# Optimization experiments

Hardware: AMD Instinct MI355X
Metric: run time of the kernel (lower is better)

The kernel has to match this reference:

```python
import jax, jax.numpy as jnp
import numpy as np

B, T, C = 2, 2048, 2048
H, KVH, HD = 16, 4, 128  # heads, kv heads, head_dim
G = H // KVH             # GQA group size
THETA = 10000.0


def _rope_cos_sin(t, hd, dtype):
    inv_freq = 1.0 / (THETA ** (jnp.arange(0, hd, 2, dtype=jnp.float32) / hd))
    pos = jnp.arange(t, dtype=jnp.float32)
    freqs = pos[:, None] * inv_freq[None, :]          # [T, hd/2]
    emb = jnp.concatenate([freqs, freqs], axis=-1)    # [T, hd]
    return jnp.cos(emb).astype(dtype), jnp.sin(emb).astype(dtype)


def _rotate_half(x):
    x1, x2 = jnp.split(x, 2, axis=-1)
    return jnp.concatenate([-x2, x1], axis=-1)


def setup_inputs() -> dict:
    key = jax.random.key(0)
    ks = jax.random.split(key, 5)
    s_in = 1.0 / np.sqrt(C)
    return {
        "x": jax.random.normal(ks[0], (B, T, C), jnp.float32),
        "wq": jax.random.normal(ks[1], (C, H * HD), jnp.float32) * s_in,
        "bq": jnp.zeros((H * HD,), jnp.float32),
        "wk": jax.random.normal(ks[2], (C, KVH * HD), jnp.float32) * s_in,
        "bk": jnp.zeros((KVH * HD,), jnp.float32),
        "wv": jax.random.normal(ks[3], (C, KVH * HD), jnp.float32) * s_in,
        "bv": jnp.zeros((KVH * HD,), jnp.float32),
        "wo": jax.random.normal(ks[4], (H * HD, C), jnp.float32) * (1.0 / np.sqrt(H * HD)),
    }


def reference(x, wq, bq, wk, bk, wv, bv, wo):
    b, t, c = x.shape
    q = (x @ wq + bq).reshape(b, t, H, HD).transpose(0, 2, 1, 3)    # [B,H,T,hd]
    k = (x @ wk + bk).reshape(b, t, KVH, HD).transpose(0, 2, 1, 3)  # [B,KVH,T,hd]
    v = (x @ wv + bv).reshape(b, t, KVH, HD).transpose(0, 2, 1, 3)

    cos, sin = _rope_cos_sin(t, HD, x.dtype)  # [T,hd]
    q = q * cos + _rotate_half(q) * sin
    k = k * cos + _rotate_half(k) * sin

    # GQA: group query heads over kv heads
    qg = q.reshape(b, KVH, G, t, HD)
    scale = 1.0 / np.sqrt(HD)
    scores = jnp.einsum('bkgtd,bksd->bkgts', qg, k) * scale  # [B,KVH,G,T,T]
    causal = jnp.tril(jnp.ones((t, t), bool))
    scores = jnp.where(causal, scores, jnp.finfo(scores.dtype).min)
    attn = jax.nn.softmax(scores, axis=-1)
    out = jnp.einsum('bkgts,bksd->bkgtd', attn, v)            # [B,KVH,G,T,hd]
    out = out.reshape(b, H, t, HD).transpose(0, 2, 1, 3).reshape(b, t, H * HD)
    return out @ wo
```

## Files before the change

### kernel.cpp

```cpp
#include <hip/hip_runtime.h>
#include <hip/hip_bf16.h>
#include <math.h>

#define B_ 2
#define T_ 2048
#define C_ 2048
#define H_ 16
#define KVH_ 4
#define HD_ 128
#define G_ (H_ / KVH_)
#define MROWS (B_ * T_)
#define NQKV (H_ * HD_ + 2 * KVH_ * HD_)
#define KOFF (H_ * HD_)
#define VOFF (H_ * HD_ + KVH_ * HD_)

typedef __hip_bfloat16 bf16;
typedef short bf16x8 __attribute__((ext_vector_type(8)));
typedef short bf16x4 __attribute__((ext_vector_type(4)));
typedef float f32x4 __attribute__((ext_vector_type(4)));

__device__ __forceinline__ void gload_lds16(const void* g, void* l) {
  __builtin_amdgcn_global_load_lds(
      (const __attribute__((address_space(1))) unsigned int*)g,
      (__attribute__((address_space(3))) unsigned int*)l, 16, 0, 0);
}

static __device__ __forceinline__ f32x4 mfma32k(bf16x8 a, bf16x8 b, f32x4 c) {
  return __builtin_amdgcn_mfma_f32_16x16x32_bf16(a, b, c, 0, 0, 0);
}

static __device__ __forceinline__ f32x4 mfma16(bf16x4 a, bf16x4 b, f32x4 c) {
#if __has_builtin(__builtin_amdgcn_mfma_f32_16x16x16_bf16)
  return __builtin_amdgcn_mfma_f32_16x16x16_bf16(a, b, c, 0, 0, 0);
#else
  return __builtin_amdgcn_mfma_f32_16x16x16bf16_1k(a, b, c, 0, 0, 0);
#endif
}

static __device__ __forceinline__ short f2bf(float x) {
  unsigned u = __builtin_bit_cast(unsigned, x);
  u += 0x7FFFu + ((u >> 16) & 1u);
  return (short)(u >> 16);
}

static __device__ __forceinline__ float fexp2(float x) {
#if __has_builtin(__builtin_amdgcn_exp2f)
  return __builtin_amdgcn_exp2f(x);
#else
  return exp2f(x);
#endif
}

__global__ void cast_bf16_kernel(const float* __restrict__ in, bf16* __restrict__ out, int n) {
  int i = (blockIdx.x * 256 + threadIdx.x) * 4;
  if (i >= n) return;
  float4 v = *(const float4*)(in + i);
  out[i + 0] = __float2bfloat16(v.x);
  out[i + 1] = __float2bfloat16(v.y);
  out[i + 2] = __float2bfloat16(v.z);
  out[i + 3] = __float2bfloat16(v.w);
}

__global__ __launch_bounds__(256) void transpose_cast(const float* __restrict__ in,
                                                      bf16* __restrict__ out,
                                                      int R, int Ccols) {
  __shared__ float t[32][33];
  const int tx = threadIdx.x & 31, ty = threadIdx.x >> 5;
  const int r0 = blockIdx.y * 32, c0 = blockIdx.x * 32;
#pragma unroll
  for (int it = 0; it < 4; ++it)
    t[ty + 8 * it][tx] = in[(size_t)(r0 + ty + 8 * it) * Ccols + c0 + tx];
  __syncthreads();
#pragma unroll
  for (int it = 0; it < 4; ++it)
    out[(size_t)(c0 + ty + 8 * it) * R + r0 + tx] = __float2bfloat16(t[tx][ty + 8 * it]);
}

__global__ __launch_bounds__(256) void transpose_cast_qkvw(
    const float* __restrict__ wq, const float* __restrict__ wk,
    const float* __restrict__ wv, bf16* __restrict__ outT) {
  __shared__ float t[32][33];
  const int tx = threadIdx.x & 31, ty = threadIdx.x >> 5;
  const int r0 = blockIdx.y * 32;
  const int c0 = blockIdx.x * 32;
  const float* src;
  int nn, ld;
  if (c0 < KOFF)      { src = wq; nn = c0;        ld = 2048; }
  else if (c0 < VOFF) { src = wk; nn = c0 - KOFF; ld = 512; }
  else                { src = wv; nn = c0 - VOFF; ld = 512; }
#pragma unroll
  for (int it = 0; it < 4; ++it)
    t[ty + 8 * it][tx] = src[(size_t)(r0 + ty + 8 * it) * ld + nn + tx];
  __syncthreads();
#pragma unroll
  for (int it = 0; it < 4; ++it)
    outT[(size_t)(c0 + ty + 8 * it) * 2048 + r0 + tx] = __float2bfloat16(t[tx][ty + 8 * it]);
}

__global__ void rope_bf16(bf16* __restrict__ buf) {
  const int row = blockIdx.x / 20;
  const int hh = blockIdx.x % 20;
  const int t = row % T_;
  const int d = threadIdx.x;
  bf16* rp = buf + (size_t)row * NQKV + hh * HD_;
  float vd = __bfloat162float(rp[d]);
  float vp = __bfloat162float(rp[d ^ 64]);
  __syncthreads();
  const int i = d & 63;
  float invf = fexp2(-(float)i * (13.287712379549449f / 64.0f));
  float ang = (float)t * invf;
  float s, c;
  __sincosf(ang, &s, &c);
  rp[d] = __float2bfloat16((d < 64) ? (vd * c - vp * s) : (vd * c + vp * s));
}

__global__ __launch_bounds__(256) void pack_k(const bf16* __restrict__ qkv,
                                              bf16* __restrict__ kp) {
  const int tile = blockIdx.x & 63;
  const int bk = blockIdx.x >> 6;
  const int b = bk >> 2, kvh = bk & 3;
#pragma unroll
  for (int u = 0; u < 2; ++u) {
    const int t = threadIdx.x + u * 256;
    const int kc = t >> 6, L = t & 63;
    const bf16* src = qkv +
        (size_t)(b * T_ + tile * 32 + 16 * (kc >> 2) + (L & 15)) * NQKV +
        KOFF + kvh * HD_ + (kc & 3) * 32 + (L >> 4) * 8;
    bf16x8 v = *(const bf16x8*)src;
    *(bf16x8*)(kp + ((size_t)(bk * 64 + tile) * 8 + kc) * 512 + L * 8) = v;
  }
}

__global__ __launch_bounds__(256) void pack_v(const bf16* __restrict__ qkv,
                                              bf16* __restrict__ vp) {
  const int tile = blockIdx.x & 63;
  const int bk = blockIdx.x >> 6;
  const int b = bk >> 2, kvh = bk & 3;
#pragma unroll
  for (int u = 0; u < 2; ++u) {
    const int t = threadIdx.x + u * 256;
    const int ht = t >> 6, L = t & 63;
    const int colL = L & 15, quad = L >> 4;
    const bf16* base = qkv + (size_t)(b * T_ + tile * 32 + quad * 4) * NQKV +
                       VOFF + kvh * HD_ + ht * 16 + colL;
    bf16x8 v;
#pragma unroll
    for (int j = 0; j < 4; ++j) {
      v[j]     = *(const short*)(base + (size_t)j * NQKV);
      v[j + 4] = *(const short*)(base + (size_t)(16 + j) * NQKV);
    }
    *(bf16x8*)(vp + ((size_t)(bk * 64 + tile) * 8 + ht) * 512 + L * 8) = v;
  }
}

template <bool BF16OUT>
__global__ __launch_bounds__(256, 2) void gemm_mfma(
    const bf16* __restrict__ A, const bf16* __restrict__ Bt, void* __restrict__ Cout,
    const float* __restrict__ bq, const float* __restrict__ bk2,
    const float* __restrict__ bv2, int M, int N, int K) {
  __shared__ __align__(16) bf16 As[128 * 32];
  __shared__ __align__(16) bf16 Bs[128 * 32];
  const int tid = threadIdx.x;
  const int w = tid >> 6, lane = tid & 63;
  const int colL = lane & 15, quad = lane >> 4;
  const int wm = w & 1, wn = w >> 1;
  const int r0 = blockIdx.y * 128, c0 = blockIdx.x * 128;

  f32x4 acc[4][4];
  const f32x4 zero = {0.f, 0.f, 0.f, 0.f};
#pragma unroll
  for (int mt = 0; mt < 4; ++mt)
#pragma unroll
    for (int nt = 0; nt < 4; ++nt) acc[mt][nt] = zero;

  for (int k0 = 0; k0 < K; k0 += 32) {
    __syncthreads();
#pragma unroll
    for (int it = 0; it < 2; ++it) {
      const int seg = it * 4 + w;
      const int idx = seg * 64 + lane;
      const int row = idx >> 2, off = idx & 3;
      gload_lds16(A + (size_t)(r0 + row) * K + k0 + off * 8, &As[seg * 512]);
      gload_lds16(Bt + (size_t)(c0 + row) * K + k0 + off * 8, &Bs[seg * 512]);
    }
    __syncthreads();
    bf16x8 af[4], bfv[4];
#pragma unroll
    for (int mt = 0; mt < 4; ++mt)
      af[mt] = *(const bf16x8*)&As[(wm * 64 + mt * 16 + colL) * 32 + quad * 8];
#pragma unroll
    for (int nt = 0; nt < 4; ++nt)
      bfv[nt] = *(const bf16x8*)&Bs[(wn * 64 + nt * 16 + colL) * 32 + quad * 8];
#pragma unroll
    for (int mt = 0; mt < 4; ++mt)
#pragma unroll
      for (int nt = 0; nt < 4; ++nt)
        acc[mt][nt] =
            __builtin_amdgcn_mfma_f32_16x16x32_bf16(af[mt], bfv[nt], acc[mt][nt], 0, 0, 0);
  }

#pragma unroll
  for (int nt = 0; nt < 4; ++nt) {
    const int c = c0 + wn * 64 + nt * 16 + colL;
    float bias = 0.f;
    if (bq) bias = (c < KOFF) ? bq[c] : (c < VOFF ? bk2[c - KOFF] : bv2[c - VOFF]);
#pragma unroll
    for (int mt = 0; mt < 4; ++mt) {
#pragma unroll
      for (int i = 0; i < 4; ++i) {
        const int r = r0 + wm * 64 + mt * 16 + quad * 4 + i;
        const float v = acc[mt][nt][i] + bias;
        if (BF16OUT)
          ((bf16*)Cout)[(size_t)r * N + c] = __float2bfloat16(v);
        else
          ((float*)Cout)[(size_t)r * N + c] = v;
      }
    }
  }
}

#define FA_SCL2 (0.08838834764831845f * 1.4426950408889634f)
#define FA_M2 16.0f

__global__ __launch_bounds__(256, 2) void flash_mfma8(
    const bf16* __restrict__ qkv, const bf16* __restrict__ kp,
    const bf16* __restrict__ vp, bf16* __restrict__ ao) {
  __shared__ __align__(16) bf16 KS[3][4096];
  __shared__ __align__(16) bf16 VS[3][4096];

  const int id = blockIdx.x;
  const int bk = id & 7;
  const int u = id >> 3;
  const int j = (u < 32) ? (63 - u) : (u - 32);
  const int b = bk >> 2, kvh = bk & 3;
  const int w = threadIdx.x >> 6;
  const int h = (kvh << 2) | w;
  const int lane = threadIdx.x & 63;
  const int colL = lane & 15, quad = lane >> 4;
  const int myq0 = j * 32;
  const int nkv = j + 1;

  const bf16* kpt = kp + ((size_t)(bk * 64)) * 4096 + (w * 2) * 512 + lane * 8;
  const bf16* vpt = vp + ((size_t)(bk * 64)) * 4096 + (w * 2) * 512 + lane * 8;

  auto stageK = [&](int tile, int slot) {
    const bf16* s = kpt + (size_t)tile * 4096;
    bf16* d = &KS[slot][(w * 2) * 512];
    gload_lds16(s, d);
    gload_lds16(s + 512, d + 512);
  };
  auto stageV = [&](int tile, int slot) {
    const bf16* s = vpt + (size_t)tile * 4096;
    bf16* d = &VS[slot][(w * 2) * 512];
    gload_lds16(s, d);
    gload_lds16(s + 512, d + 512);
  };

  bf16x8 qf[2][4];
  {
    const bf16* qg = qkv + (size_t)(b * T_ + myq0) * NQKV + h * HD_;
#pragma unroll
    for (int mq = 0; mq < 2; ++mq)
#pragma unroll
      for (int c = 0; c < 4; ++c)
        qf[mq][c] = *(const bf16x8*)(qg + (size_t)(mq * 16 + colL) * NQKV + c * 32 + quad * 8);
  }

  const f32x4 zero = {0.f, 0.f, 0.f, 0.f};
  auto qk = [&](const bf16* Kb, f32x4 (&s_)[2][2]) {
    s_[0][0] = zero; s_[0][1] = zero; s_[1][0] = zero; s_[1][1] = zero;
#pragma unroll
    for (int c = 0; c < 4; ++c) {
      bf16x8 kf0 = *(const bf16x8*)(Kb + c * 512 + lane * 8);
      bf16x8 kf1 = *(const bf16x8*)(Kb + (4 + c) * 512 + lane * 8);
#pragma unroll
      for (int mq = 0; mq < 2; ++mq) {
        s_[0][mq] = mfma32k(kf0, qf[mq][c], s_[0][mq]);
        s_[1][mq] = mfma32k(kf1, qf[mq][c], s_[1][mq]);
      }
    }
  };

  f32x4 o[2][8];
#pragma unroll
  for (int mq = 0; mq < 2; ++mq)
#pragma unroll
    for (int ht = 0; ht < 8; ++ht) o[mq][ht] = zero;
  float l_[2] = {0.f, 0.f};

  stageK(0, 0);
  if (nkv > 1) stageK(1, 1);
  if (nkv > 2) stageK(2, 2);
  stageV(0, 0);
  if (nkv > 1) stageV(1, 1);
  asm volatile("s_waitcnt vmcnt(0)\n\ts_barrier" ::: "memory");

  f32x4 sA[2][2], sB[2][2];
  qk(KS[0], sA);

  int kStage = 0, kNext = 1, vRead = 0, vStage = 2;
#pragma unroll 1
  for (int tt = 0; tt < nkv; ++tt) {
    const bool sk = (tt + 3 < nkv), sv = (tt + 2 < nkv);
    if (sk) stageK(tt + 3, kStage);
    if (sv) stageV(tt + 2, vStage);

    if (tt + 1 < nkv) qk(KS[kNext], sB);

    bf16x4 pf[2][2];
    if (tt == nkv - 1) {
#pragma unroll
      for (int kt = 0; kt < 2; ++kt)
#pragma unroll
        for (int mq = 0; mq < 2; ++mq) {
          const int qc = mq * 16 + colL;
          const int kb = kt * 16 + quad * 4;
          float pv[4];
#pragma unroll
          for (int i = 0; i < 4; ++i) {
            float e = fexp2(fmaf(sA[kt][mq][i], FA_SCL2, -FA_M2));
            pv[i] = (kb + i <= qc) ? e : 0.f;
          }
          l_[mq] += (pv[0] + pv[1]) + (pv[2] + pv[3]);
          pf[kt][mq] = (bf16x4){f2bf(pv[0]), f2bf(pv[1]), f2bf(pv[2]), f2bf(pv[3])};
        }
    } else {
#pragma unroll
      for (int kt = 0; kt < 2; ++kt)
#pragma unroll
        for (int mq = 0; mq < 2; ++mq) {
          float pv[4];
#pragma unroll
          for (int i = 0; i < 4; ++i)
            pv[i] = fexp2(fmaf(sA[kt][mq][i], FA_SCL2, -FA_M2));
          l_[mq] += (pv[0] + pv[1]) + (pv[2] + pv[3]);
          pf[kt][mq] = (bf16x4){f2bf(pv[0]), f2bf(pv[1]), f2bf(pv[2]), f2bf(pv[3])};
        }
    }

    {
      const bf16* Vb = VS[vRead];
#pragma unroll
      for (int ht = 0; ht < 8; ++ht) {
        bf16x8 vf8 = *(const bf16x8*)(Vb + ht * 512 + lane * 8);
        bf16x4 lo = __builtin_shufflevector(vf8, vf8, 0, 1, 2, 3);
        bf16x4 hi = __builtin_shufflevector(vf8, vf8, 4, 5, 6, 7);
#pragma unroll
        for (int mq = 0; mq < 2; ++mq) {
          o[mq][ht] = mfma16(lo, pf[0][mq], o[mq][ht]);
          o[mq][ht] = mfma16(hi, pf[1][mq], o[mq][ht]);
        }
      }
    }

    if (sk)      asm volatile("s_waitcnt vmcnt(4)\n\ts_barrier" ::: "memory");
    else if (sv) asm volatile("s_waitcnt vmcnt(2)\n\ts_barrier" ::: "memory");
    else         asm volatile("s_waitcnt vmcnt(0)\n\ts_barrier" ::: "memory");

#pragma unroll
    for (int a = 0; a < 2; ++a)
#pragma unroll
      for (int bb = 0; bb < 2; ++bb) sA[a][bb] = sB[a][bb];
    kStage = (kStage == 2) ? 0 : kStage + 1;
    kNext  = (kNext == 2) ? 0 : kNext + 1;
    vRead  = (vRead == 2) ? 0 : vRead + 1;
    vStage = (vStage == 2) ? 0 : vStage + 1;
  }

#pragma unroll
  for (int mq = 0; mq < 2; ++mq) {
    float lv = l_[mq];
    lv += __shfl_xor(lv, 16);
    lv += __shfl_xor(lv, 32);
    const float rl = 1.f / lv;
    const size_t rbase = (size_t)(b * T_ + myq0 + mq * 16 + colL) * (H_ * HD_) + h * HD_;
#pragma unroll
    for (int ht = 0; ht < 8; ++ht) {
      bf16x4 ov;
#pragma unroll
      for (int i = 0; i < 4; ++i) ov[i] = f2bf(o[mq][ht][i] * rl);
      *(bf16x4*)(ao + rbase + ht * 16 + quad * 4) = ov;
    }
  }
}

extern "C" void kernel_launch(void* const* d_in, const int* in_sizes, int n_in,
                              void* d_out, int out_size, void* d_ws, size_t ws_size,
                              hipStream_t stream) {
  (void)in_sizes; (void)n_in; (void)out_size; (void)ws_size;
  const float* x  = (const float*)d_in[0];
  const float* wq = (const float*)d_in[1];
  const float* bq = (const float*)d_in[2];
  const float* wk = (const float*)d_in[3];
  const float* bk = (const float*)d_in[4];
  const float* wv = (const float*)d_in[5];
  const float* bv = (const float*)d_in[6];
  const float* wo = (const float*)d_in[7];
  float* out = (float*)d_out;

  char* ws = (char*)d_ws;
  bf16* xb    = (bf16*)ws;
  bf16* wqkvT = (bf16*)(ws + (16u << 20));
  bf16* woT   = (bf16*)(ws + (28u << 20));
  bf16* qkv   = (bf16*)(ws + (36u << 20));
  bf16* kp    = (bf16*)(ws + (60u << 20));
  bf16* vp    = (bf16*)(ws + (68u << 20));

  cast_bf16_kernel<<<dim3(MROWS * C_ / 1024), dim3(256), 0, stream>>>(x, xb, MROWS * C_);

  transpose_cast_qkvw<<<dim3(96, 64), dim3(256), 0, stream>>>(wq, wk, wv, wqkvT);
  transpose_cast<<<dim3(64, 64), dim3(256), 0, stream>>>(wo, woT, 2048, 2048);

  gemm_mfma<true><<<dim3(NQKV / 128, MROWS / 128), dim3(256), 0, stream>>>(
      xb, wqkvT, qkv, bq, bk, bv, MROWS, NQKV, C_);

  rope_bf16<<<dim3(MROWS * 20), dim3(128), 0, stream>>>(qkv);

  pack_k<<<dim3(8 * 64), dim3(256), 0, stream>>>(qkv, kp);
  pack_v<<<dim3(8 * 64), dim3(256), 0, stream>>>(qkv, vp);

  bf16* ao = xb;
  flash_mfma8<<<dim3(512), dim3(256), 0, stream>>>(qkv, kp, vp, ao);

  gemm_mfma<false><<<dim3(C_ / 128, MROWS / 128), dim3(256), 0, stream>>>(
      ao, woT, out, nullptr, nullptr, nullptr, MROWS, C_, KOFF);
}
```

Measured before the change: 345.6 us.

## Add 256-row, 4-stage pipelined GEMM and raise wave priority around MFMA

Adds a new GEMM kernel with 512-thread blocks and 256-row tiles. It uses a 4-deep LDS ring fed by direct global-to-LDS loads and splits each K step into two MFMA halves, with barriers and s_setprio around each half. The QKV projection uses 256x256 tiles and the output projection uses 256x128 tiles. The flash-attention MFMA sections also get s_setprio raised. The aim is more operand reuse per load and better overlap of loads with MFMA, at the cost of more LDS and registers per block, fewer blocks in flight, and added barriers.

```diff
diff --git a/kernel.cpp b/kernel.cpp
--- a/kernel.cpp
+++ b/kernel.cpp
@@ -219,6 +219,130 @@
   }
 }
 
+template <bool BF16OUT, int NF>
+__global__ __launch_bounds__(512, 2) void gemm_mfma256(
+    const bf16* __restrict__ A, const bf16* __restrict__ Bt, void* __restrict__ Cout,
+    const float* __restrict__ bq, const float* __restrict__ bk2,
+    const float* __restrict__ bv2, int M, int N, int K) {
+  constexpr int BN = NF * 64;
+  constexpr int LB = BN / 128;
+  __shared__ __align__(16) bf16 As[4][256 * 32];
+  __shared__ __align__(16) bf16 Bs[4][BN * 32];
+
+  const int tid = threadIdx.x;
+  const int w = tid >> 6, lane = tid & 63;
+  const int colL = lane & 15, quad = lane >> 4;
+  const int wm = w >> 2, wn = w & 3;
+  const int r0 = blockIdx.y * 256, c0 = blockIdx.x * BN;
+  const int sq = (quad ^ (colL & 3)) * 8;
+  const int srow = lane >> 2;
+  const int ssl = ((lane & 3) ^ (srow & 3)) * 8;
+  const int nk = K >> 5;
+
+  auto stageA = [&](int kt, int bi, int it) {
+    const int row = (it * 8 + w) * 16 + srow;
+    gload_lds16(A + (size_t)(r0 + row) * K + (kt << 5) + ssl,
+                &As[bi][(it * 8 + w) * 512]);
+  };
+  auto stageB = [&](int kt, int bi, int it) {
+    const int row = (it * 8 + w) * 16 + srow;
+    gload_lds16(Bt + (size_t)(c0 + row) * K + (kt << 5) + ssl,
+                &Bs[bi][(it * 8 + w) * 512]);
+  };
+
+  f32x4 acc[8][NF];
+  const f32x4 zero = {0.f, 0.f, 0.f, 0.f};
+#pragma unroll
+  for (int m = 0; m < 8; ++m)
+#pragma unroll
+    for (int n = 0; n < NF; ++n) acc[m][n] = zero;
+
+#pragma unroll
+  for (int pt = 0; pt < 3; ++pt) {
+    stageA(pt, pt, 0); stageA(pt, pt, 1);
+    stageB(pt, pt, 0);
+    if constexpr (LB == 2) stageB(pt, pt, 1);
+  }
+  if constexpr (LB == 2)
+    asm volatile("s_waitcnt vmcnt(8)\n\ts_barrier" ::: "memory");
+  else
+    asm volatile("s_waitcnt vmcnt(6)\n\ts_barrier" ::: "memory");
+
+#pragma unroll 1
+  for (int t = 0; t < nk; ++t) {
+    const int bi = t & 3, sbi = (t + 3) & 3;
+    const bool st = (t + 3 < nk);
+
+    bf16x8 a0[4], b0[NF], a1[4];
+#pragma unroll
+    for (int m = 0; m < 4; ++m)
+      a0[m] = *(const bf16x8*)&As[bi][(wm * 128 + m * 16 + colL) * 32 + sq];
+#pragma unroll
+    for (int n = 0; n < NF; ++n)
+      b0[n] = *(const bf16x8*)&Bs[bi][(wn * (NF * 16) + n * 16 + colL) * 32 + sq];
+    if (st) { stageA(t + 3, sbi, 0); stageA(t + 3, sbi, 1); }
+    __builtin_amdgcn_s_barrier();
+    __builtin_amdgcn_s_setprio(1);
+#pragma unroll
+    for (int m = 0; m < 4; ++m)
+#pragma unroll
+      for (int n = 0; n < NF; ++n)
+        acc[m][n] = mfma32k(a0[m], b0[n], acc[m][n]);
+    __builtin_amdgcn_s_setprio(0);
+    __builtin_amdgcn_s_barrier();
+
+#pragma unroll
+    for (int m = 0; m < 4; ++m)
+      a1[m] = *(const bf16x8*)&As[bi][(wm * 128 + (m + 4) * 16 + colL) * 32 + sq];
+    if (st) {
+      stageB(t + 3, sbi, 0);
+      if constexpr (LB == 2) stageB(t + 3, sbi, 1);
+    }
+    if (st) {
+      if constexpr (LB == 2)
+        asm volatile("s_waitcnt vmcnt(8)\n\ts_barrier" ::: "memory");
+      else
+        asm volatile("s_waitcnt vmcnt(6)\n\ts_barrier" ::: "memory");
+    } else if (t + 2 < nk) {
+      if constexpr (LB == 2)
+        asm volatile("s_waitcnt vmcnt(4)\n\ts_barrier" ::: "memory");
+      else
+        asm volatile("s_waitcnt vmcnt(3)\n\ts_barrier" ::: "memory");
+    } else if (t + 1 < nk) {
+      asm volatile("s_waitcnt vmcnt(0)\n\ts_barrier" ::: "memory");
+    } else {
+      __builtin_amdgcn_s_barrier();
+    }
+    __builtin_amdgcn_s_setprio(1);
+#pragma unroll
+    for (int m = 0; m < 4; ++m)
+#pragma unroll
+      for (int n = 0; n < NF; ++n)
+        acc[m + 4][n] = mfma32k(a1[m], b0[n], acc[m + 4][n]);
+    __builtin_amdgcn_s_setprio(0);
+    __builtin_amdgcn_s_barrier();
+  }
+
+#pragma unroll
+  for (int nt = 0; nt < NF; ++nt) {
+    const int c = c0 + wn * (NF * 16) + nt * 16 + colL;
+    float bias = 0.f;
+    if (bq) bias = (c < KOFF) ? bq[c] : (c < VOFF ? bk2[c - KOFF] : bv2[c - VOFF]);
+#pragma unroll
+    for (int mt = 0; mt < 8; ++mt) {
+#pragma unroll
+      for (int i = 0; i < 4; ++i) {
+        const int r = r0 + wm * 128 + mt * 16 + quad * 4 + i;
+        const float v = acc[mt][nt][i] + bias;
+        if (BF16OUT)
+          ((bf16*)Cout)[(size_t)r * N + c] = __float2bfloat16(v);
+        else
+          ((float*)Cout)[(size_t)r * N + c] = v;
+      }
+    }
+  }
+}
+
 #define FA_SCL2 (0.08838834764831845f * 1.4426950408889634f)
 #define FA_M2 16.0f
 
@@ -269,6 +393,7 @@
   const f32x4 zero = {0.f, 0.f, 0.f, 0.f};
   auto qk = [&](const bf16* Kb, f32x4 (&s_)[2][2]) {
     s_[0][0] = zero; s_[0][1] = zero; s_[1][0] = zero; s_[1][1] = zero;
+    __builtin_amdgcn_s_setprio(1);
 #pragma unroll
     for (int c = 0; c < 4; ++c) {
       bf16x8 kf0 = *(const bf16x8*)(Kb + c * 512 + lane * 8);
@@ -279,6 +404,7 @@
         s_[1][mq] = mfma32k(kf1, qf[mq][c], s_[1][mq]);
       }
     }
+    __builtin_amdgcn_s_setprio(0);
   };
 
   f32x4 o[2][8];
@@ -340,6 +466,7 @@
 
     {
       const bf16* Vb = VS[vRead];
+      __builtin_amdgcn_s_setprio(1);
 #pragma unroll
       for (int ht = 0; ht < 8; ++ht) {
         bf16x8 vf8 = *(const bf16x8*)(Vb + ht * 512 + lane * 8);
@@ -351,6 +478,7 @@
           o[mq][ht] = mfma16(hi, pf[1][mq], o[mq][ht]);
         }
       }
+      __builtin_amdgcn_s_setprio(0);
     }
 
     if (sk)      asm volatile("s_waitcnt vmcnt(4)\n\ts_barrier" ::: "memory");
@@ -411,7 +539,7 @@
   transpose_cast_qkvw<<<dim3(96, 64), dim3(256), 0, stream>>>(wq, wk, wv, wqkvT);
   transpose_cast<<<dim3(64, 64), dim3(256), 0, stream>>>(wo, woT, 2048, 2048);
 
-  gemm_mfma<true><<<dim3(NQKV / 128, MROWS / 128), dim3(256), 0, stream>>>(
+  gemm_mfma256<true, 4><<<dim3(NQKV / 256, MROWS / 256), dim3(512), 0, stream>>>(
       xb, wqkvT, qkv, bq, bk, bv, MROWS, NQKV, C_);
 
   rope_bf16<<<dim3(MROWS * 20), dim3(128), 0, stream>>>(qkv);
@@ -422,6 +550,6 @@
   bf16* ao = xb;
   flash_mfma8<<<dim3(512), dim3(256), 0, stream>>>(qkv, kp, vp, ao);
 
-  gemm_mfma<false><<<dim3(C_ / 128, MROWS / 128), dim3(256), 0, stream>>>(
+  gemm_mfma256<false, 2><<<dim3(C_ / 128, MROWS / 256), dim3(512), 0, stream>>>(
       ao, woT, out, nullptr, nullptr, nullptr, MROWS, C_, KOFF);
 }
```

Measured after the change: 360.7 us. 1.04x slower.

## Halve flash-attention query tile to 16 rows and double the grid

Applied to the files above, without the earlier changes.

Each flash-attention block now handles 16 query rows per head instead of 32, so the grid grows from 512 to 1024 blocks. Blocks are ordered longest-first, and launch bounds rise to 3 blocks per CU. The aim is more parallelism and better occupancy and load balance across CUs. The cost is that each K/V tile is loaded from global memory and LDS twice as often per query row, and there are fewer MFMAs per LDS read.

```diff
diff --git a/kernel.cpp b/kernel.cpp
--- a/kernel.cpp
+++ b/kernel.cpp
@@ -222,7 +222,7 @@
 #define FA_SCL2 (0.08838834764831845f * 1.4426950408889634f)
 #define FA_M2 16.0f
 
-__global__ __launch_bounds__(256, 2) void flash_mfma8(
+__global__ __launch_bounds__(256, 3) void flash_mfma8(
     const bf16* __restrict__ qkv, const bf16* __restrict__ kp,
     const bf16* __restrict__ vp, bf16* __restrict__ ao) {
   __shared__ __align__(16) bf16 KS[3][4096];
@@ -231,14 +231,14 @@
   const int id = blockIdx.x;
   const int bk = id & 7;
   const int u = id >> 3;
-  const int j = (u < 32) ? (63 - u) : (u - 32);
+  const int jq = 127 - u;
   const int b = bk >> 2, kvh = bk & 3;
   const int w = threadIdx.x >> 6;
   const int h = (kvh << 2) | w;
   const int lane = threadIdx.x & 63;
   const int colL = lane & 15, quad = lane >> 4;
-  const int myq0 = j * 32;
-  const int nkv = j + 1;
+  const int myq0 = jq * 16;
+  const int nkv = (jq >> 1) + 1;
 
   const bf16* kpt = kp + ((size_t)(bk * 64)) * 4096 + (w * 2) * 512 + lane * 8;
   const bf16* vpt = vp + ((size_t)(bk * 64)) * 4096 + (w * 2) * 512 + lane * 8;
@@ -256,37 +256,30 @@
     gload_lds16(s + 512, d + 512);
   };
 
-  bf16x8 qf[2][4];
+  bf16x8 qf[4];
   {
     const bf16* qg = qkv + (size_t)(b * T_ + myq0) * NQKV + h * HD_;
 #pragma unroll
-    for (int mq = 0; mq < 2; ++mq)
-#pragma unroll
-      for (int c = 0; c < 4; ++c)
-        qf[mq][c] = *(const bf16x8*)(qg + (size_t)(mq * 16 + colL) * NQKV + c * 32 + quad * 8);
+    for (int c = 0; c < 4; ++c)
+      qf[c] = *(const bf16x8*)(qg + (size_t)colL * NQKV + c * 32 + quad * 8);
   }
 
   const f32x4 zero = {0.f, 0.f, 0.f, 0.f};
-  auto qk = [&](const bf16* Kb, f32x4 (&s_)[2][2]) {
-    s_[0][0] = zero; s_[0][1] = zero; s_[1][0] = zero; s_[1][1] = zero;
+  auto qk = [&](const bf16* Kb, f32x4 (&s_)[2]) {
+    s_[0] = zero; s_[1] = zero;
 #pragma unroll
     for (int c = 0; c < 4; ++c) {
       bf16x8 kf0 = *(const bf16x8*)(Kb + c * 512 + lane * 8);
       bf16x8 kf1 = *(const bf16x8*)(Kb + (4 + c) * 512 + lane * 8);
-#pragma unroll
-      for (int mq = 0; mq < 2; ++mq) {
-        s_[0][mq] = mfma32k(kf0, qf[mq][c], s_[0][mq]);
-        s_[1][mq] = mfma32k(kf1, qf[mq][c], s_[1][mq]);
-      }
+      s_[0] = mfma32k(kf0, qf[c], s_[0]);
+      s_[1] = mfma32k(kf1, qf[c], s_[1]);
     }
   };
 
-  f32x4 o[2][8];
-#pragma unroll
-  for (int mq = 0; mq < 2; ++mq)
-#pragma unroll
-    for (int ht = 0; ht < 8; ++ht) o[mq][ht] = zero;
-  float l_[2] = {0.f, 0.f};
+  f32x4 o[8];
+#pragma unroll
+  for (int ht = 0; ht < 8; ++ht) o[ht] = zero;
+  float l_ = 0.f;
 
   stageK(0, 0);
   if (nkv > 1) stageK(1, 1);
@@ -295,7 +288,7 @@
   if (nkv > 1) stageV(1, 1);
   asm volatile("s_waitcnt vmcnt(0)\n\ts_barrier" ::: "memory");
 
-  f32x4 sA[2][2], sB[2][2];
+  f32x4 sA[2], sB[2];
   qk(KS[0], sA);
 
   int kStage = 0, kNext = 1, vRead = 0, vStage = 2;
@@ -307,35 +300,31 @@
 
     if (tt + 1 < nkv) qk(KS[kNext], sB);
 
-    bf16x4 pf[2][2];
+    bf16x4 pf[2];
     if (tt == nkv - 1) {
-#pragma unroll
-      for (int kt = 0; kt < 2; ++kt)
-#pragma unroll
-        for (int mq = 0; mq < 2; ++mq) {
-          const int qc = mq * 16 + colL;
-          const int kb = kt * 16 + quad * 4;
-          float pv[4];
-#pragma unroll
-          for (int i = 0; i < 4; ++i) {
-            float e = fexp2(fmaf(sA[kt][mq][i], FA_SCL2, -FA_M2));
-            pv[i] = (kb + i <= qc) ? e : 0.f;
-          }
-          l_[mq] += (pv[0] + pv[1]) + (pv[2] + pv[3]);
-          pf[kt][mq] = (bf16x4){f2bf(pv[0]), f2bf(pv[1]), f2bf(pv[2]), f2bf(pv[3])};
+      const int qg = ((jq & 1) << 4) | colL;
+#pragma unroll
+      for (int kt = 0; kt < 2; ++kt) {
+        const int kb = kt * 16 + quad * 4;
+        float pv[4];
+#pragma unroll
+        for (int i = 0; i < 4; ++i) {
+          float e = fexp2(fmaf(sA[kt][i], FA_SCL2, -FA_M2));
+          pv[i] = (kb + i <= qg) ? e : 0.f;
         }
+        l_ += (pv[0] + pv[1]) + (pv[2] + pv[3]);
+        pf[kt] = (bf16x4){f2bf(pv[0]), f2bf(pv[1]), f2bf(pv[2]), f2bf(pv[3])};
+      }
     } else {
 #pragma unroll
-      for (int kt = 0; kt < 2; ++kt)
-#pragma unroll
-        for (int mq = 0; mq < 2; ++mq) {
-          float pv[4];
-#pragma unroll
-          for (int i = 0; i < 4; ++i)
-            pv[i] = fexp2(fmaf(sA[kt][mq][i], FA_SCL2, -FA_M2));
-          l_[mq] += (pv[0] + pv[1]) + (pv[2] + pv[3]);
-          pf[kt][mq] = (bf16x4){f2bf(pv[0]), f2bf(pv[1]), f2bf(pv[2]), f2bf(pv[3])};
-        }
+      for (int kt = 0; kt < 2; ++kt) {
+        float pv[4];
+#pragma unroll
+        for (int i = 0; i < 4; ++i)
+          pv[i] = fexp2(fmaf(sA[kt][i], FA_SCL2, -FA_M2));
+        l_ += (pv[0] + pv[1]) + (pv[2] + pv[3]);
+        pf[kt] = (bf16x4){f2bf(pv[0]), f2bf(pv[1]), f2bf(pv[2]), f2bf(pv[3])};
+      }
     }
 
     {
@@ -345,11 +334,8 @@
         bf16x8 vf8 = *(const bf16x8*)(Vb + ht * 512 + lane * 8);
         bf16x4 lo = __builtin_shufflevector(vf8, vf8, 0, 1, 2, 3);
         bf16x4 hi = __builtin_shufflevector(vf8, vf8, 4, 5, 6, 7);
-#pragma unroll
-        for (int mq = 0; mq < 2; ++mq) {
-          o[mq][ht] = mfma16(lo, pf[0][mq], o[mq][ht]);
-          o[mq][ht] = mfma16(hi, pf[1][mq], o[mq][ht]);
-        }
+        o[ht] = mfma16(lo, pf[0], o[ht]);
+        o[ht] = mfma16(hi, pf[1], o[ht]);
       }
     }
 
@@ -357,28 +343,24 @@
     else if (sv) asm volatile("s_waitcnt vmcnt(2)\n\ts_barrier" ::: "memory");
     else         asm volatile("s_waitcnt vmcnt(0)\n\ts_barrier" ::: "memory");
 
-#pragma unroll
-    for (int a = 0; a < 2; ++a)
-#pragma unroll
-      for (int bb = 0; bb < 2; ++bb) sA[a][bb] = sB[a][bb];
+    sA[0] = sB[0]; sA[1] = sB[1];
     kStage = (kStage == 2) ? 0 : kStage + 1;
     kNext  = (kNext == 2) ? 0 : kNext + 1;
     vRead  = (vRead == 2) ? 0 : vRead + 1;
     vStage = (vStage == 2) ? 0 : vStage + 1;
   }
 
-#pragma unroll
-  for (int mq = 0; mq < 2; ++mq) {
-    float lv = l_[mq];
+  {
+    float lv = l_;
     lv += __shfl_xor(lv, 16);
     lv += __shfl_xor(lv, 32);
     const float rl = 1.f / lv;
-    const size_t rbase = (size_t)(b * T_ + myq0 + mq * 16 + colL) * (H_ * HD_) + h * HD_;
+    const size_t rbase = (size_t)(b * T_ + myq0 + colL) * (H_ * HD_) + h * HD_;
 #pragma unroll
     for (int ht = 0; ht < 8; ++ht) {
       bf16x4 ov;
 #pragma unroll
-      for (int i = 0; i < 4; ++i) ov[i] = f2bf(o[mq][ht][i] * rl);
+      for (int i = 0; i < 4; ++i) ov[i] = f2bf(o[ht][i] * rl);
       *(bf16x4*)(ao + rbase + ht * 16 + quad * 4) = ov;
     }
   }
@@ -420,7 +402,7 @@
   pack_v<<<dim3(8 * 64), dim3(256), 0, stream>>>(qkv, vp);
 
   bf16* ao = xb;
-  flash_mfma8<<<dim3(512), dim3(256), 0, stream>>>(qkv, kp, vp, ao);
+  flash_mfma8<<<dim3(1024), dim3(256), 0, stream>>>(qkv, kp, vp, ao);
 
   gemm_mfma<false><<<dim3(C_ / 128, MROWS / 128), dim3(256), 0, stream>>>(
       ao, woT, out, nullptr, nullptr, nullptr, MROWS, C_, KOFF);
```

After: 330.8 us. 1.04x faster.
